# Performance work log

Hardware: AMD Instinct MI355X
Metric: run time of the kernel (lower is better)

Reference implementation:

```python
import jax, jax.numpy as jnp
import numpy as np

N = 50000      # nodes
E = 800000     # edges
G = 256        # graphs in batch
D_IN = 128     # input_dim
H = 128        # node_hidden_dim
FC = 128       # fc_hidden_dim
OUT = 2        # out_dim
EPS = 1e-5


def _lin_init(key, fan_in, fan_out, bias=True):
    kw, kb = jax.random.split(key)
    w = jax.random.normal(kw, (fan_in, fan_out), jnp.float32) / np.sqrt(fan_in)
    if bias:
        b = jax.random.normal(kb, (fan_out,), jnp.float32) * 0.01
        return w, b
    return w


def setup_inputs() -> dict:
    key = jax.random.key(0)
    ks = jax.random.split(key, 16)
    x = jax.random.normal(ks[0], (N, D_IN), jnp.float32)
    edge_index = jax.random.randint(ks[1], (2, E), 0, N, jnp.int32)
    batch = jnp.sort(jax.random.randint(ks[2], (N,), 0, G, jnp.int32))
    edge_attr = jax.random.uniform(ks[3], (E, 1), jnp.float32)
    # GraphConv params: lin_rel (with bias) + lin_root (no bias)
    w_rel1, b_rel1 = _lin_init(ks[4], D_IN, H)
    w_root1 = _lin_init(ks[5], D_IN, H, bias=False)
    w_rel2, b_rel2 = _lin_init(ks[6], H, 2 * H)
    w_root2 = _lin_init(ks[7], H, 2 * H, bias=False)
    w_rel3, b_rel3 = _lin_init(ks[8], 2 * H, 3 * H)
    w_root3 = _lin_init(ks[9], 2 * H, 3 * H, bias=False)
    # BatchNorm affine params
    gamma1 = jnp.ones((H,), jnp.float32);      beta1 = jnp.zeros((H,), jnp.float32)
    gamma2 = jnp.ones((2 * H,), jnp.float32);  beta2 = jnp.zeros((2 * H,), jnp.float32)
    gamma3 = jnp.ones((3 * H,), jnp.float32);  beta3 = jnp.zeros((3 * H,), jnp.float32)
    # FC head: lin1 in = 3H+6H+9H = 18H
    w_lin1, b_lin1 = _lin_init(ks[10], 18 * H, FC)
    w_lin2, b_lin2 = _lin_init(ks[11], FC, OUT)
    w_lin3, b_lin3 = _lin_init(ks[12], OUT, OUT)
    return dict(x=x, edge_index=edge_index, batch=batch, edge_attr=edge_attr,
                w_rel1=w_rel1, b_rel1=b_rel1, w_root1=w_root1,
                w_rel2=w_rel2, b_rel2=b_rel2, w_root2=w_root2,
                w_rel3=w_rel3, b_rel3=b_rel3, w_root3=w_root3,
                gamma1=gamma1, beta1=beta1, gamma2=gamma2, beta2=beta2,
                gamma3=gamma3, beta3=beta3,
                w_lin1=w_lin1, b_lin1=b_lin1, w_lin2=w_lin2, b_lin2=b_lin2,
                w_lin3=w_lin3, b_lin3=b_lin3)


def _bn(h, gamma, beta):
    # training-mode BatchNorm1d over node axis
    mu = h.mean(0)
    var = h.var(0)
    return (h - mu) * jax.lax.rsqrt(var + EPS) * gamma + beta


def _gconv(h, src, dst, ew, w_rel, b_rel, w_root):
    # PyG GraphConv: lin_rel(sum_j ew_ij * x_j) + lin_root(x_i)
    agg = jax.ops.segment_sum(h[src] * ew[:, None], dst, num_segments=N)
    return agg @ w_rel + b_rel + h @ w_root


def _pool3(h, batch):
    # concat of global max / mean / add pooling per graph
    s = jax.ops.segment_sum(h, batch, num_segments=G)
    cnt = jax.ops.segment_sum(jnp.ones((h.shape[0], 1), h.dtype), batch, num_segments=G)
    mean = s / jnp.maximum(cnt, 1.0)
    m = jax.ops.segment_max(h, batch, num_segments=G)
    m = jnp.where(cnt > 0, m, 0.0)  # guard empty segments
    return jnp.concatenate([m, mean, s], axis=1)


def reference(x, edge_index, batch, edge_attr,
              w_rel1, b_rel1, w_root1, w_rel2, b_rel2, w_root2,
              w_rel3, b_rel3, w_root3,
              gamma1, beta1, gamma2, beta2, gamma3, beta3,
              w_lin1, b_lin1, w_lin2, b_lin2, w_lin3, b_lin3):
    ew = jnp.transpose(edge_attr, (1, 0))[0]            # [E]
    src, dst = edge_index[0], edge_index[1]
    h = _bn(jax.nn.leaky_relu(_gconv(x, src, dst, ew, w_rel1, b_rel1, w_root1)), gamma1, beta1)
    x1 = _pool3(h, batch)
    h = _bn(jax.nn.leaky_relu(_gconv(h, src, dst, ew, w_rel2, b_rel2, w_root2)), gamma2, beta2)
    x2 = _pool3(h, batch)
    h = _bn(jax.nn.leaky_relu(_gconv(h, src, dst, ew, w_rel3, b_rel3, w_root3)), gamma3, beta3)
    x3 = _pool3(h, batch)
    z = jnp.concatenate([x1, x2, x3], axis=1)           # [G, 18H]
    z = jax.nn.relu(z @ w_lin1 + b_lin1)                # dropout is identity in eval
    z = jax.nn.relu(z @ w_lin2 + b_lin2)
    return jax.nn.log_softmax(z @ w_lin3 + b_lin3, axis=-1)
```

## Files before the change

kernel.cpp:

```cpp
#include <hip/hip_runtime.h>
#include <cstdint>
#include <cstddef>

#define N_NODES 50000
#define M_PAD   50048
#define MB_TILES 391
#define N_EDGES 800000
#define N_GRAPH 256
#define Z_DIM   2304
#define NREP    16
#define POOL_TOT (N_GRAPH * (128 + 256 + 384))

static constexpr float LEAKY  = 0.01f;
static constexpr float BN_EPS = 1e-5f;

typedef short short8 __attribute__((ext_vector_type(8)));
typedef float floatx4 __attribute__((ext_vector_type(4)));
typedef const __attribute__((address_space(1))) unsigned int* gas_ptr;
typedef __attribute__((address_space(3))) unsigned int* las_ptr;
typedef unsigned long long ull;

__device__ __forceinline__ unsigned short f2b(float f) {
  union { float f; unsigned int u; } v; v.f = f;
  unsigned int u = v.u;
  unsigned int r = (u + 0x7FFFu + ((u >> 16) & 1u)) >> 16;
  return (unsigned short)r;
}
__device__ __forceinline__ float b2f(unsigned short h) {
  union { unsigned int u; float f; } v; v.u = ((unsigned int)h) << 16;
  return v.f;
}
__device__ __forceinline__ unsigned fkey(float x) {
  unsigned k = __float_as_uint(x);
  return k ^ ((k & 0x80000000u) ? 0xFFFFFFFFu : 0x80000000u);
}
__device__ __forceinline__ float kdec(unsigned k) {
  k ^= (k & 0x80000000u) ? 0x80000000u : 0xFFFFFFFFu;
  return __uint_as_float(k);
}


__global__ void init_all_kernel(int* __restrict__ cntR, int* __restrict__ gcnt,
                                float* __restrict__ sums_all,
                                unsigned* __restrict__ pmaxk, unsigned* __restrict__ pmink,
                                float* __restrict__ psumg) {
  const int i = blockIdx.x * blockDim.x + threadIdx.x;
  if (i < NREP * N_NODES) cntR[i] = 0;
  if (i < N_GRAPH) gcnt[i] = 0;
  if (i < 2 * (128 + 256 + 384)) sums_all[i] = 0.f;
  if (i < POOL_TOT) { pmaxk[i] = 0u; pmink[i] = 0xFFFFFFFFu; psumg[i] = 0.f; }
}


__global__ void hist_rep_kernel(const int* __restrict__ idx, int* __restrict__ cntR, int n) {
  int i = blockIdx.x * blockDim.x + threadIdx.x;
  if (i < n) {
    const int rep = blockIdx.x & (NREP - 1);
    atomicAdd(&cntR[rep * N_NODES + idx[i]], 1);
  }
}

__global__ __launch_bounds__(256) void scan1_fused_kernel(int* __restrict__ cntR,
                                                          int* __restrict__ out,
                                                          int* __restrict__ part, int n) {
  __shared__ int sm[256];
  const int t = threadIdx.x;
  const int base = blockIdx.x * 1024 + t * 4;
  int v[4] = {0, 0, 0, 0};
#pragma unroll
  for (int j = 0; j < 4; ++j) {
    const int d = base + j;
    if (d < n) {
      int s = 0;
#pragma unroll
      for (int r = 0; r < NREP; ++r) {
        const int c = cntR[r * N_NODES + d];
        cntR[r * N_NODES + d] = s;
        s += c;
      }
      v[j] = s;
    }
  }
  const int tsum = v[0] + v[1] + v[2] + v[3];
  sm[t] = tsum;
  __syncthreads();
  for (int off = 1; off < 256; off <<= 1) {
    int x = (t >= off) ? sm[t - off] : 0;
    __syncthreads();
    sm[t] += x;
    __syncthreads();
  }
  const int excl = sm[t] - tsum;
  if (base     < n) out[base]     = excl;
  if (base + 1 < n) out[base + 1] = excl + v[0];
  if (base + 2 < n) out[base + 2] = excl + v[0] + v[1];
  if (base + 3 < n) out[base + 3] = excl + v[0] + v[1] + v[2];
  if (t == 255) part[blockIdx.x] = sm[255];
}

__global__ __launch_bounds__(256) void scan2_kernel(int* __restrict__ part, int nb,
                                                    int* __restrict__ total_out) {
  __shared__ int sm[256];
  const int t = threadIdx.x;
  const int v = (t < nb) ? part[t] : 0;
  sm[t] = v;
  __syncthreads();
  for (int off = 1; off < 256; off <<= 1) {
    int x = (t >= off) ? sm[t - off] : 0;
    __syncthreads();
    sm[t] += x;
    __syncthreads();
  }
  if (t < nb) part[t] = sm[t] - v;
  if (t == 255) *total_out = sm[255];
}

__global__ void scan3_cursor_kernel(int* __restrict__ out, const int* __restrict__ part,
                                    int* __restrict__ cntR, int n) {
  int i = blockIdx.x * blockDim.x + threadIdx.x;
  if (i >= n) return;
  const int rp = out[i] + part[i >> 10];
  out[i] = rp;
#pragma unroll
  for (int r = 0; r < NREP; ++r) cntR[r * N_NODES + i] += rp;
}

__global__ void bucket_kernel(const int* __restrict__ src, const int* __restrict__ dst,
                              const float* __restrict__ ew, int* __restrict__ cntR,
                              ull* __restrict__ epack, int E) {
  int e = blockIdx.x * blockDim.x + threadIdx.x;
  if (e < E) {
    const int rep = blockIdx.x & (NREP - 1);
    const int d = dst[e];
    const int p = atomicAdd(&cntR[rep * N_NODES + d], 1);
    epack[p] = ((ull)__float_as_uint(ew[e]) << 32) | (unsigned)src[e];
  }
}

__global__ __launch_bounds__(256) void hist_batch_kernel(const int* __restrict__ idx,
                                                         int* __restrict__ cnt, int n) {
  __shared__ int lh[N_GRAPH];
  lh[threadIdx.x] = 0;
  __syncthreads();
  int i = blockIdx.x * blockDim.x + threadIdx.x;
  if (i < n) atomicAdd(&lh[idx[i]], 1);
  __syncthreads();
  const int v = lh[threadIdx.x];
  if (v) atomicAdd(&cnt[threadIdx.x], v);
}

__global__ __launch_bounds__(256) void scan256_kernel(const int* __restrict__ cnt,
                                                      int* __restrict__ gptr) {
  __shared__ int sm[256];
  const int t = threadIdx.x;
  const int v = cnt[t];
  sm[t] = v;
  __syncthreads();
  for (int off = 1; off < 256; off <<= 1) {
    int x = (t >= off) ? sm[t - off] : 0;
    __syncthreads();
    sm[t] += x;
    __syncthreads();
  }
  gptr[t] = sm[t] - v;
  if (t == 255) gptr[256] = sm[255];
}


__global__ void cast_bf16_kernel(const float* __restrict__ in,
                                 unsigned short* __restrict__ out, int npair) {
  int i = blockIdx.x * blockDim.x + threadIdx.x;
  if (i >= npair) return;
  float2 v = *(const float2*)(in + 2 * (size_t)i);
  ((unsigned int*)out)[i] = (unsigned int)f2b(v.x) | ((unsigned int)f2b(v.y) << 16);
}

__global__ __launch_bounds__(256) void wt_build_kernel(
    const float* __restrict__ wrel, const float* __restrict__ wroot,
    const float* __restrict__ brel, const float* __restrict__ sums_prev,
    const float* __restrict__ gamma_prev, const float* __restrict__ beta_prev,
    unsigned short* __restrict__ wt, float* __restrict__ u, float* __restrict__ v,
    int K, int N) {
  __shared__ float redu[256];
  __shared__ float redv[256];
  const int n = blockIdx.x;
  const int K2 = 2 * K;
  const float inv_n = 1.f / (float)N_NODES;
  float us = 0.f, vs = 0.f;
  for (int k = threadIdx.x; k < K2; k += 256) {
    const int kk = (k < K) ? k : k - K;
    const float w = (k < K) ? wrel[(size_t)kk * N + n] : wroot[(size_t)kk * N + n];
    float sc = 1.f, sh = 0.f;
    if (sums_prev) {
      const float mu  = sums_prev[kk] * inv_n;
      const float var = sums_prev[K + kk] * inv_n - mu * mu;
      sc = rsqrtf(var + BN_EPS) * gamma_prev[kk];
      sh = beta_prev[kk] - mu * sc;
    }
    wt[(size_t)n * K2 + k] = f2b(w * sc);
    if (k < K) us += sh * w; else vs += sh * w;
  }
  redu[threadIdx.x] = us; redv[threadIdx.x] = vs;
  __syncthreads();
  for (int o = 128; o > 0; o >>= 1) {
    if (threadIdx.x < o) {
      redu[threadIdx.x] += redu[threadIdx.x + o];
      redv[threadIdx.x] += redv[threadIdx.x + o];
    }
    __syncthreads();
  }
  if (threadIdx.x == 0) { u[n] = redu[0]; v[n] = brel[n] + redv[0]; }
}


template <int D>
__global__ void agg_bf16_kernel(const unsigned short* __restrict__ h,
                                const int* __restrict__ rowptr,
                                const ull* __restrict__ epack,
                                unsigned short* __restrict__ agg,
                                float* __restrict__ degw_out) {
  int gid  = blockIdx.x * blockDim.x + threadIdx.x;
  int node = gid >> 6;
  int lane = threadIdx.x & 63;
  if (node >= N_NODES) return;
  const int beg = rowptr[node], end = rowptr[node + 1];
  constexpr int NP = D / 128;
  float acc0[NP], acc1[NP];
#pragma unroll
  for (int i = 0; i < NP; ++i) { acc0[i] = 0.f; acc1[i] = 0.f; }
  float wsum = 0.f;

  for (int c0 = beg; c0 < end; c0 += 64) {
    const int cn = min(64, end - c0);
    ull pk = 0;
    if (lane < cn) pk = epack[c0 + lane];
    const int   su = (int)(unsigned)pk;
    const float wf = __uint_as_float((unsigned)(pk >> 32));
    const int ng = (cn + 7) >> 3;
    for (int g = 0; g < ng; ++g) {
      int ss[8]; float wv[8];
#pragma unroll
      for (int j = 0; j < 8; ++j) {
        ss[j] = __shfl(su, g * 8 + j);
        wv[j] = __shfl(wf, g * 8 + j);
      }
      unsigned uu[8][NP];
#pragma unroll
      for (int j = 0; j < 8; ++j) {
        const unsigned int* row = (const unsigned int*)(h + (size_t)ss[j] * D);
#pragma unroll
        for (int i = 0; i < NP; ++i) uu[j][i] = row[lane + 64 * i];
      }
#pragma unroll
      for (int j = 0; j < 8; ++j) {
        wsum += wv[j];
#pragma unroll
        for (int i = 0; i < NP; ++i) {
          acc0[i] += b2f((unsigned short)(uu[j][i] & 0xFFFF)) * wv[j];
          acc1[i] += b2f((unsigned short)(uu[j][i] >> 16)) * wv[j];
        }
      }
    }
  }

  unsigned int* o = (unsigned int*)(agg + (size_t)node * D);
#pragma unroll
  for (int i = 0; i < NP; ++i)
    o[lane + 64 * i] = (unsigned int)f2b(acc0[i]) | ((unsigned int)f2b(acc1[i]) << 16);
  if (degw_out != nullptr && lane == 0) degw_out[node] = wsum;
}


__global__ __launch_bounds__(256) void gemm_mfma_kernel(
    const unsigned short* __restrict__ Aagg, const unsigned short* __restrict__ Ah,
    const unsigned short* __restrict__ Wt,
    const float* __restrict__ u, const float* __restrict__ v,
    const float* __restrict__ degw,
    unsigned short* __restrict__ outH, float* __restrict__ sums,
    int M, int K, int N) {
  __shared__ unsigned short As[3][128 * 32];
  __shared__ unsigned short Bs[3][128 * 32];
  __shared__ float col_s[256];
  __shared__ float dws[128];

  const int NT = N >> 7;
  const int id = blockIdx.x;
  const int xcd = id & 7;
  const int q   = id >> 3;
  const int m_tile = (q / NT) * 8 + xcd;
  if (m_tile >= MB_TILES) return;
  const int m0 = m_tile * 128;
  const int n0 = (q % NT) * 128;

  const int t  = threadIdx.x;
  const int lane = t & 63;
  const int w    = t >> 6;
  const int wm   = (w & 1) * 64;
  const int wn   = (w >> 1) * 64;
  const int l16  = lane & 15;
  const int lq   = lane >> 4;
  const int K2   = 2 * K;

  const int lrow  = lane >> 2;
  const int lslot = lane & 3;

  col_s[t] = 0.f;
  if (t < 128) {
    const int m = m0 + t;
    dws[t] = (m < M) ? degw[m] : 0.f;
  }

  floatx4 acc[4][4];
#pragma unroll
  for (int i = 0; i < 4; ++i)
#pragma unroll
    for (int j = 0; j < 4; ++j) acc[i][j] = (floatx4){0.f, 0.f, 0.f, 0.f};

  auto stage = [&](unsigned short* Ab, unsigned short* Bb, int k0) {
    const unsigned short* Asrc;
    int kbase;
    if (k0 < K) { Asrc = Aagg; kbase = k0; } else { Asrc = Ah; kbase = k0 - K; }
#pragma unroll
    for (int qq = 0; qq < 2; ++qq) {
      const int row = w * 32 + qq * 16 + lrow;
      const int gc  = (lslot ^ ((row >> 1) & 3)) * 8;
      const unsigned short* gA = Asrc + (size_t)(m0 + row) * K + kbase + gc;
      const unsigned short* gB = Wt + (size_t)(n0 + row) * K2 + k0 + gc;
      __builtin_amdgcn_global_load_lds((gas_ptr)gA, (las_ptr)(Ab + (w * 32 + qq * 16) * 32),
                                       16, 0, 0);
      __builtin_amdgcn_global_load_lds((gas_ptr)gB, (las_ptr)(Bb + (w * 32 + qq * 16) * 32),
                                       16, 0, 0);
    }
  };

  auto compute = [&](const unsigned short* Ab, const unsigned short* Bb) {
    short8 af[4], bfr[4];
#pragma unroll
    for (int i = 0; i < 4; ++i) {
      const int r = wm + i * 16 + l16;
      af[i] = *(const short8*)(Ab + r * 32 + (lq ^ ((r >> 1) & 3)) * 8);
    }
#pragma unroll
    for (int j = 0; j < 4; ++j) {
      const int r = wn + j * 16 + l16;
      bfr[j] = *(const short8*)(Bb + r * 32 + (lq ^ ((r >> 1) & 3)) * 8);
    }
    __builtin_amdgcn_s_setprio(1);
#pragma unroll
    for (int i = 0; i < 4; ++i)
#pragma unroll
      for (int j = 0; j < 4; ++j)
        acc[i][j] = __builtin_amdgcn_mfma_f32_16x16x32_bf16(af[i], bfr[j], acc[i][j], 0, 0, 0);
    __builtin_amdgcn_s_setprio(0);
  };

  const int NSTEP = K2 >> 5;

  unsigned short *A0 = &As[0][0], *A1 = &As[1][0], *A2 = &As[2][0];
  unsigned short *B0 = &Bs[0][0], *B1 = &Bs[1][0], *B2 = &Bs[2][0];

  stage(A0, B0, 0);
  stage(A1, B1, 1 << 5);

  for (int s = 0; s < NSTEP - 1; ++s) {
    asm volatile("s_waitcnt vmcnt(4)" ::: "memory");
    __builtin_amdgcn_s_barrier();
    __builtin_amdgcn_sched_barrier(0);
    if (s + 2 < NSTEP) stage(A2, B2, (s + 2) << 5);
    compute(A0, B0);
    unsigned short* tA = A0; A0 = A1; A1 = A2; A2 = tA;
    unsigned short* tB = B0; B0 = B1; B1 = B2; B2 = tB;
  }
  asm volatile("s_waitcnt vmcnt(0)" ::: "memory");
  __builtin_amdgcn_s_barrier();
  __builtin_amdgcn_sched_barrier(0);
  compute(A0, B0);

  float uu[4], vv[4];
#pragma unroll
  for (int j = 0; j < 4; ++j) {
    const int n = n0 + wn + j * 16 + l16;
    uu[j] = u[n]; vv[j] = v[n];
  }

  float ts[4]  = {0.f, 0.f, 0.f, 0.f};
  float tss[4] = {0.f, 0.f, 0.f, 0.f};
#pragma unroll
  for (int i = 0; i < 4; ++i) {
    const int lrow2 = wm + i * 16 + lq * 4;
#pragma unroll
    for (int j = 0; j < 4; ++j) {
      const int n = n0 + wn + j * 16 + l16;
#pragma unroll
      for (int r = 0; r < 4; ++r) {
        const int m = m0 + lrow2 + r;
        if (m < M) {
          float val = acc[i][j][r] + vv[j] + dws[lrow2 + r] * uu[j];
          val = val > 0.f ? val : LEAKY * val;
          outH[(size_t)m * N + n] = f2b(val);
          ts[j]  += val;
          tss[j] += val * val;
        }
      }
    }
  }
#pragma unroll
  for (int j = 0; j < 4; ++j) {
    float a = ts[j], b = tss[j];
    a += __shfl_xor(a, 16); a += __shfl_xor(a, 32);
    b += __shfl_xor(b, 16); b += __shfl_xor(b, 32);
    if (lq == 0) {
      const int ci = wn + j * 16 + l16;
      atomicAdd(&col_s[ci], a);
      atomicAdd(&col_s[128 + ci], b);
    }
  }
  __syncthreads();
  if (t < 128) {
    atomicAdd(&sums[n0 + t], col_s[t]);
    atomicAdd(&sums[N + n0 + t], col_s[128 + t]);
  }
}


__global__ void pool_bf16_kernel(const unsigned short* __restrict__ hp,
                                 const int* __restrict__ batch,
                                 unsigned* __restrict__ pmaxk, unsigned* __restrict__ pmink,
                                 float* __restrict__ psumg, int n, int C) {
  __shared__ int bs[64];
  const int tc = threadIdx.x;
  const int r0 = blockIdx.x * 64;
  const int r1 = min(n, r0 + 64);
  if (tc < 64 && r0 + tc < n) bs[tc] = batch[r0 + tc];
  __syncthreads();
  int cur_g = bs[0];
  float mx0 = -3.4e38f, mn0 = 3.4e38f, s0 = 0.f;
  float mx1 = -3.4e38f, mn1 = 3.4e38f, s1 = 0.f;
  for (int r = r0; r < r1; ++r) {
    const int g = bs[r - r0];
    if (g != cur_g) {
      const int c0 = 2 * tc;
      atomicMax(&pmaxk[(size_t)cur_g * C + c0], fkey(mx0));
      atomicMin(&pmink[(size_t)cur_g * C + c0], fkey(mn0));
      atomicAdd(&psumg[(size_t)cur_g * C + c0], s0);
      atomicMax(&pmaxk[(size_t)cur_g * C + c0 + 1], fkey(mx1));
      atomicMin(&pmink[(size_t)cur_g * C + c0 + 1], fkey(mn1));
      atomicAdd(&psumg[(size_t)cur_g * C + c0 + 1], s1);
      mx0 = -3.4e38f; mn0 = 3.4e38f; s0 = 0.f;
      mx1 = -3.4e38f; mn1 = 3.4e38f; s1 = 0.f;
      cur_g = g;
    }
    const unsigned uu = ((const unsigned*)(hp + (size_t)r * C))[tc];
    const float a = b2f((unsigned short)(uu & 0xFFFF));
    const float b = b2f((unsigned short)(uu >> 16));
    mx0 = fmaxf(mx0, a); mn0 = fminf(mn0, a); s0 += a;
    mx1 = fmaxf(mx1, b); mn1 = fminf(mn1, b); s1 += b;
  }
  const int c0 = 2 * tc;
  atomicMax(&pmaxk[(size_t)cur_g * C + c0], fkey(mx0));
  atomicMin(&pmink[(size_t)cur_g * C + c0], fkey(mn0));
  atomicAdd(&psumg[(size_t)cur_g * C + c0], s0);
  atomicMax(&pmaxk[(size_t)cur_g * C + c0 + 1], fkey(mx1));
  atomicMin(&pmink[(size_t)cur_g * C + c0 + 1], fkey(mn1));
  atomicAdd(&psumg[(size_t)cur_g * C + c0 + 1], s1);
}


__global__ void pool_finalize_all_kernel(const unsigned* __restrict__ pmaxk,
                                         const unsigned* __restrict__ pmink,
                                         const float* __restrict__ psumg,
                                         const float* __restrict__ sums_all,
                                         const float* __restrict__ gamma1, const float* __restrict__ beta1,
                                         const float* __restrict__ gamma2, const float* __restrict__ beta2,
                                         const float* __restrict__ gamma3, const float* __restrict__ beta3,
                                         const int* __restrict__ gptr,
                                         float* __restrict__ z) {
  int i = blockIdx.x * blockDim.x + threadIdx.x;
  if (i >= POOL_TOT) return;
  int C, zoff, li;
  const float *sums, *gamma, *beta;
  if (i < N_GRAPH * 128) {
    C = 128; zoff = 0; li = i;
    sums = sums_all; gamma = gamma1; beta = beta1;
  } else if (i < N_GRAPH * (128 + 256)) {
    C = 256; zoff = 384; li = i - N_GRAPH * 128;
    sums = sums_all + 2 * 128; gamma = gamma2; beta = beta2;
  } else {
    C = 384; zoff = 1152; li = i - N_GRAPH * (128 + 256);
    sums = sums_all + 2 * (128 + 256); gamma = gamma3; beta = beta3;
  }
  const int g = li / C, c = li % C;
  const int cnt = gptr[g + 1] - gptr[g];
  const float inv_n = 1.f / (float)N_NODES;
  const float mu  = sums[c] * inv_n;
  const float var = sums[C + c] * inv_n - mu * mu;
  const float sc  = rsqrtf(var + BN_EPS) * gamma[c];
  const float sh  = beta[c] - mu * sc;
  const float mx = kdec(pmaxk[i]);
  const float mn = kdec(pmink[i]);
  const float sm = psumg[i];
  const float zmax = (sc >= 0.f ? mx : mn) * sc + sh;
  const float zsum = sm * sc + (float)cnt * sh;
  float* zg = z + (size_t)g * Z_DIM + zoff;
  zg[c]         = (cnt > 0) ? zmax : 0.f;
  zg[C + c]     = zsum / (float)(cnt > 0 ? cnt : 1);
  zg[2 * C + c] = zsum;
}


__global__ __launch_bounds__(1024) void fc_kernel(const float* __restrict__ z,
                                                  const float* __restrict__ w1, const float* __restrict__ b1,
                                                  const float* __restrict__ w2, const float* __restrict__ b2,
                                                  const float* __restrict__ w3, const float* __restrict__ b3,
                                                  float* __restrict__ out) {
  __shared__ float zs[Z_DIM];
  __shared__ float part[8][128];
  __shared__ float h1s[128];
  __shared__ float red[128][2];
  __shared__ float y2[2];
  const int g  = blockIdx.x;
  const int t  = threadIdx.x;
  const int c  = t & 127;
  const int ks = t >> 7;
  for (int i = t; i < Z_DIM; i += 1024) zs[i] = z[(size_t)g * Z_DIM + i];
  __syncthreads();

  constexpr int KCH = Z_DIM / 8;
  const int k0 = ks * KCH;
  float acc = 0.f;
#pragma unroll 4
  for (int k = k0; k < k0 + KCH; ++k) acc += zs[k] * w1[(size_t)k * 128 + c];
  part[ks][c] = acc;
  __syncthreads();

  if (t < 128) {
    float s = b1[t];
#pragma unroll
    for (int i = 0; i < 8; ++i) s += part[i][t];
    h1s[t] = fmaxf(s, 0.f);
  }
  __syncthreads();
  if (t < 128) {
    red[t][0] = h1s[t] * w2[t * 2 + 0];
    red[t][1] = h1s[t] * w2[t * 2 + 1];
  }
  __syncthreads();
  if (t < 2) {
    float s = b2[t];
    for (int k = 0; k < 128; ++k) s += red[k][t];
    y2[t] = fmaxf(s, 0.f);
  }
  __syncthreads();
  if (t == 0) {
    const float z0 = y2[0] * w3[0] + y2[1] * w3[2] + b3[0];
    const float z1 = y2[0] * w3[1] + y2[1] * w3[3] + b3[1];
    const float m  = fmaxf(z0, z1);
    const float lse = m + logf(expf(z0 - m) + expf(z1 - m));
    out[g * 2 + 0] = z0 - lse;
    out[g * 2 + 1] = z1 - lse;
  }
}


extern "C" void kernel_launch(void* const* d_in, const int* in_sizes, int n_in,
                              void* d_out, int out_size, void* d_ws, size_t ws_size,
                              hipStream_t stream) {
  (void)in_sizes; (void)n_in; (void)out_size; (void)ws_size;
  const float* x        = (const float*)d_in[0];
  const int*   eidx     = (const int*)d_in[1];
  const int*   batch    = (const int*)d_in[2];
  const float* eattr    = (const float*)d_in[3];
  const float* w_rel1   = (const float*)d_in[4];
  const float* b_rel1   = (const float*)d_in[5];
  const float* w_root1  = (const float*)d_in[6];
  const float* w_rel2   = (const float*)d_in[7];
  const float* b_rel2   = (const float*)d_in[8];
  const float* w_root2  = (const float*)d_in[9];
  const float* w_rel3   = (const float*)d_in[10];
  const float* b_rel3   = (const float*)d_in[11];
  const float* w_root3  = (const float*)d_in[12];
  const float* gamma1   = (const float*)d_in[13];
  const float* beta1    = (const float*)d_in[14];
  const float* gamma2   = (const float*)d_in[15];
  const float* beta2    = (const float*)d_in[16];
  const float* gamma3   = (const float*)d_in[17];
  const float* beta3    = (const float*)d_in[18];
  const float* w_lin1   = (const float*)d_in[19];
  const float* b_lin1   = (const float*)d_in[20];
  const float* w_lin2   = (const float*)d_in[21];
  const float* b_lin2   = (const float*)d_in[22];
  const float* w_lin3   = (const float*)d_in[23];
  const float* b_lin3   = (const float*)d_in[24];

  const int* src = eidx;
  const int* dst = eidx + N_EDGES;
  float* outp = (float*)d_out;

  char* ws = (char*)d_ws;
  size_t off = 0;
  auto alloc = [&](size_t bytes) -> void* {
    void* p = ws + off;
    off += (bytes + 255) & ~(size_t)255;
    return p;
  };
  int*   rowptr = (int*)alloc((N_NODES + 1) * sizeof(int));
  int*   cntR   = (int*)alloc((size_t)NREP * N_NODES * sizeof(int));
  int*   gptr   = (int*)alloc((N_GRAPH + 1) * sizeof(int));
  int*   gcnt   = (int*)alloc(N_GRAPH * sizeof(int));
  int*   part   = (int*)alloc(256 * sizeof(int));
  ull*   epack  = (ull*)alloc((size_t)N_EDGES * sizeof(ull));
  float* degw   = (float*)alloc(N_NODES * sizeof(float));
  float* sums_all = (float*)alloc(2 * (128 + 256 + 384) * sizeof(float));
  float* zbuf   = (float*)alloc((size_t)N_GRAPH * Z_DIM * sizeof(float));
  unsigned* pmaxk = (unsigned*)alloc((size_t)POOL_TOT * 4);
  unsigned* pmink = (unsigned*)alloc((size_t)POOL_TOT * 4);
  float*    psumg = (float*)alloc((size_t)POOL_TOT * 4);
  unsigned short* xb   = (unsigned short*)alloc((size_t)M_PAD * 128 * 2);
  unsigned short* hp1  = (unsigned short*)alloc((size_t)M_PAD * 128 * 2);
  unsigned short* hp2  = (unsigned short*)alloc((size_t)M_PAD * 256 * 2);
  unsigned short* hp3  = (unsigned short*)alloc((size_t)M_PAD * 384 * 2);
  unsigned short* aggb = (unsigned short*)alloc((size_t)M_PAD * 256 * 2);
  unsigned short* wt1 = (unsigned short*)alloc((size_t)128 * 256 * 2);
  unsigned short* wt2 = (unsigned short*)alloc((size_t)256 * 256 * 2);
  unsigned short* wt3 = (unsigned short*)alloc((size_t)384 * 512 * 2);
  float* u1 = (float*)alloc(128 * sizeof(float));
  float* v1 = (float*)alloc(128 * sizeof(float));
  float* u2 = (float*)alloc(256 * sizeof(float));
  float* v2 = (float*)alloc(256 * sizeof(float));
  float* u3 = (float*)alloc(384 * sizeof(float));
  float* v3 = (float*)alloc(384 * sizeof(float));

  float* sums1 = sums_all;
  float* sums2 = sums_all + 2 * 128;
  float* sums3 = sums_all + 2 * (128 + 256);
  const int PO1 = 0, PO2 = N_GRAPH * 128, PO3 = N_GRAPH * (128 + 256);

  const int EB = (N_EDGES + 255) / 256;
  const int NB = (N_NODES + 255) / 256;
  const int RB = (N_NODES + 63) / 64;
  const int SB = (N_NODES + 1023) / 1024;

  init_all_kernel<<<(NREP * N_NODES + 255) / 256, 256, 0, stream>>>(
      cntR, gcnt, sums_all, pmaxk, pmink, psumg);

  hist_rep_kernel<<<EB, 256, 0, stream>>>(dst, cntR, N_EDGES);
  scan1_fused_kernel<<<SB, 256, 0, stream>>>(cntR, rowptr, part, N_NODES);
  scan2_kernel<<<1, 256, 0, stream>>>(part, SB, rowptr + N_NODES);
  scan3_cursor_kernel<<<NB, 256, 0, stream>>>(rowptr, part, cntR, N_NODES);
  bucket_kernel<<<EB, 256, 0, stream>>>(src, dst, eattr, cntR, epack, N_EDGES);

  hist_batch_kernel<<<NB, 256, 0, stream>>>(batch, gcnt, N_NODES);
  scan256_kernel<<<1, 256, 0, stream>>>(gcnt, gptr);

  cast_bf16_kernel<<<(N_NODES * 128 / 2 + 255) / 256, 256, 0, stream>>>(x, xb, N_NODES * 128 / 2);
  wt_build_kernel<<<128, 256, 0, stream>>>(w_rel1, w_root1, b_rel1, nullptr, nullptr, nullptr,
                                           wt1, u1, v1, 128, 128);

  const int aggBlocks = (N_NODES * 64 + 255) / 256;

  agg_bf16_kernel<128><<<aggBlocks, 256, 0, stream>>>(xb, rowptr, epack, aggb, degw);
  gemm_mfma_kernel<<<392 * 1, 256, 0, stream>>>(aggb, xb, wt1, u1, v1, degw,
                                                hp1, sums1, N_NODES, 128, 128);
  pool_bf16_kernel<<<RB, 64, 0, stream>>>(hp1, batch, pmaxk + PO1, pmink + PO1, psumg + PO1,
                                          N_NODES, 128);
  wt_build_kernel<<<256, 256, 0, stream>>>(w_rel2, w_root2, b_rel2, sums1, gamma1, beta1,
                                           wt2, u2, v2, 128, 256);

  agg_bf16_kernel<128><<<aggBlocks, 256, 0, stream>>>(hp1, rowptr, epack, aggb, nullptr);
  gemm_mfma_kernel<<<392 * 2, 256, 0, stream>>>(aggb, hp1, wt2, u2, v2, degw,
                                                hp2, sums2, N_NODES, 128, 256);
  pool_bf16_kernel<<<RB, 128, 0, stream>>>(hp2, batch, pmaxk + PO2, pmink + PO2, psumg + PO2,
                                           N_NODES, 256);
  wt_build_kernel<<<384, 256, 0, stream>>>(w_rel3, w_root3, b_rel3, sums2, gamma2, beta2,
                                           wt3, u3, v3, 256, 384);

  agg_bf16_kernel<256><<<aggBlocks, 256, 0, stream>>>(hp2, rowptr, epack, aggb, nullptr);
  gemm_mfma_kernel<<<392 * 3, 256, 0, stream>>>(aggb, hp2, wt3, u3, v3, degw,
                                                hp3, sums3, N_NODES, 256, 384);
  pool_bf16_kernel<<<RB, 192, 0, stream>>>(hp3, batch, pmaxk + PO3, pmink + PO3, psumg + PO3,
                                           N_NODES, 384);

  pool_finalize_all_kernel<<<(POOL_TOT + 255) / 256, 256, 0, stream>>>(
      pmaxk, pmink, psumg, sums_all, gamma1, beta1, gamma2, beta2, gamma3, beta3, gptr, zbuf);
  fc_kernel<<<N_GRAPH, 1024, 0, stream>>>(zbuf, w_lin1, b_lin1, w_lin2, b_lin2, w_lin3, b_lin3,
                                          outp);
}
```

Measured before the change: 560.0 us.

## Fuse segment max/min/sum pooling into GEMM epilogue and skip layer-3 output store

Moves the per-graph max/min/sum pooling into the GEMM epilogue. Each tile loops over the graph ids spanned by its 128 rows, reduces across lanes with shuffles, and issues atomics. This removes the three separate pool kernels and their re-read of the hidden activations. The third layer's activations are no longer written to memory at all, since only pooling and BN stats consume them. The cost is extra epilogue work per graph segment in each tile and more register pressure in the GEMM.

```diff
diff --git a/kernel.cpp b/kernel.cpp
--- a/kernel.cpp
+++ b/kernel.cpp
@@ -275,13 +275,16 @@
     const unsigned short* __restrict__ Aagg, const unsigned short* __restrict__ Ah,
     const unsigned short* __restrict__ Wt,
     const float* __restrict__ u, const float* __restrict__ v,
-    const float* __restrict__ degw,
+    const float* __restrict__ degw, const int* __restrict__ batch,
     unsigned short* __restrict__ outH, float* __restrict__ sums,
+    unsigned* __restrict__ pmaxk, unsigned* __restrict__ pmink,
+    float* __restrict__ psumg,
     int M, int K, int N) {
   __shared__ unsigned short As[3][128 * 32];
   __shared__ unsigned short Bs[3][128 * 32];
   __shared__ float col_s[256];
   __shared__ float dws[128];
+  __shared__ int gbs[128];
 
   const int NT = N >> 7;
   const int id = blockIdx.x;
@@ -308,6 +311,7 @@
   if (t < 128) {
     const int m = m0 + t;
     dws[t] = (m < M) ? degw[m] : 0.f;
+    gbs[t] = (m < M) ? batch[m] : -1;
   }
 
   floatx4 acc[4][4];
@@ -383,6 +387,7 @@
     uu[j] = u[n]; vv[j] = v[n];
   }
 
+  const bool wout = (outH != nullptr);
   float ts[4]  = {0.f, 0.f, 0.f, 0.f};
   float tss[4] = {0.f, 0.f, 0.f, 0.f};
 #pragma unroll
@@ -397,7 +402,7 @@
         if (m < M) {
           float val = acc[i][j][r] + vv[j] + dws[lrow2 + r] * uu[j];
           val = val > 0.f ? val : LEAKY * val;
-          outH[(size_t)m * N + n] = f2b(val);
+          if (wout) outH[(size_t)m * N + n] = f2b(val);
           ts[j]  += val;
           tss[j] += val * val;
         }
@@ -415,54 +420,45 @@
       atomicAdd(&col_s[128 + ci], b);
     }
   }
+
+  const int lastr = min(127, M - 1 - m0);
+  const int gmin = gbs[0];
+  const int gmax = gbs[lastr];
+  for (int g = gmin; g <= gmax; ++g) {
+#pragma unroll
+    for (int j = 0; j < 4; ++j) {
+      float mx = -3.4e38f, mn = 3.4e38f, sm = 0.f;
+#pragma unroll
+      for (int i = 0; i < 4; ++i) {
+        const int lrow2 = wm + i * 16 + lq * 4;
+#pragma unroll
+        for (int r = 0; r < 4; ++r) {
+          const int row = lrow2 + r;
+          const int m = m0 + row;
+          if (m < M && gbs[row] == g) {
+            float val = acc[i][j][r] + vv[j] + dws[row] * uu[j];
+            val = val > 0.f ? val : LEAKY * val;
+            mx = fmaxf(mx, val); mn = fminf(mn, val); sm += val;
+          }
+        }
+      }
+      mx = fmaxf(mx, __shfl_xor(mx, 16)); mx = fmaxf(mx, __shfl_xor(mx, 32));
+      mn = fminf(mn, __shfl_xor(mn, 16)); mn = fminf(mn, __shfl_xor(mn, 32));
+      sm += __shfl_xor(sm, 16); sm += __shfl_xor(sm, 32);
+      if (lq == 0 && mx > -3.3e38f) {
+        const size_t pi = (size_t)g * N + (n0 + wn + j * 16 + l16);
+        atomicMax(&pmaxk[pi], fkey(mx));
+        atomicMin(&pmink[pi], fkey(mn));
+        atomicAdd(&psumg[pi], sm);
+      }
+    }
+  }
+
   __syncthreads();
   if (t < 128) {
     atomicAdd(&sums[n0 + t], col_s[t]);
     atomicAdd(&sums[N + n0 + t], col_s[128 + t]);
   }
-}
-
-
-__global__ void pool_bf16_kernel(const unsigned short* __restrict__ hp,
-                                 const int* __restrict__ batch,
-                                 unsigned* __restrict__ pmaxk, unsigned* __restrict__ pmink,
-                                 float* __restrict__ psumg, int n, int C) {
-  __shared__ int bs[64];
-  const int tc = threadIdx.x;
-  const int r0 = blockIdx.x * 64;
-  const int r1 = min(n, r0 + 64);
-  if (tc < 64 && r0 + tc < n) bs[tc] = batch[r0 + tc];
-  __syncthreads();
-  int cur_g = bs[0];
-  float mx0 = -3.4e38f, mn0 = 3.4e38f, s0 = 0.f;
-  float mx1 = -3.4e38f, mn1 = 3.4e38f, s1 = 0.f;
-  for (int r = r0; r < r1; ++r) {
-    const int g = bs[r - r0];
-    if (g != cur_g) {
-      const int c0 = 2 * tc;
-      atomicMax(&pmaxk[(size_t)cur_g * C + c0], fkey(mx0));
-      atomicMin(&pmink[(size_t)cur_g * C + c0], fkey(mn0));
-      atomicAdd(&psumg[(size_t)cur_g * C + c0], s0);
-      atomicMax(&pmaxk[(size_t)cur_g * C + c0 + 1], fkey(mx1));
-      atomicMin(&pmink[(size_t)cur_g * C + c0 + 1], fkey(mn1));
-      atomicAdd(&psumg[(size_t)cur_g * C + c0 + 1], s1);
-      mx0 = -3.4e38f; mn0 = 3.4e38f; s0 = 0.f;
-      mx1 = -3.4e38f; mn1 = 3.4e38f; s1 = 0.f;
-      cur_g = g;
-    }
-    const unsigned uu = ((const unsigned*)(hp + (size_t)r * C))[tc];
-    const float a = b2f((unsigned short)(uu & 0xFFFF));
-    const float b = b2f((unsigned short)(uu >> 16));
-    mx0 = fmaxf(mx0, a); mn0 = fminf(mn0, a); s0 += a;
-    mx1 = fmaxf(mx1, b); mn1 = fminf(mn1, b); s1 += b;
-  }
-  const int c0 = 2 * tc;
-  atomicMax(&pmaxk[(size_t)cur_g * C + c0], fkey(mx0));
-  atomicMin(&pmink[(size_t)cur_g * C + c0], fkey(mn0));
-  atomicAdd(&psumg[(size_t)cur_g * C + c0], s0);
-  atomicMax(&pmaxk[(size_t)cur_g * C + c0 + 1], fkey(mx1));
-  atomicMin(&pmink[(size_t)cur_g * C + c0 + 1], fkey(mn1));
-  atomicAdd(&psumg[(size_t)cur_g * C + c0 + 1], s1);
 }
 
 
@@ -618,7 +614,6 @@
   unsigned short* xb   = (unsigned short*)alloc((size_t)M_PAD * 128 * 2);
   unsigned short* hp1  = (unsigned short*)alloc((size_t)M_PAD * 128 * 2);
   unsigned short* hp2  = (unsigned short*)alloc((size_t)M_PAD * 256 * 2);
-  unsigned short* hp3  = (unsigned short*)alloc((size_t)M_PAD * 384 * 2);
   unsigned short* aggb = (unsigned short*)alloc((size_t)M_PAD * 256 * 2);
   unsigned short* wt1 = (unsigned short*)alloc((size_t)128 * 256 * 2);
   unsigned short* wt2 = (unsigned short*)alloc((size_t)256 * 256 * 2);
@@ -637,7 +632,6 @@
 
   const int EB = (N_EDGES + 255) / 256;
   const int NB = (N_NODES + 255) / 256;
-  const int RB = (N_NODES + 63) / 64;
   const int SB = (N_NODES + 1023) / 1024;
 
   init_all_kernel<<<(NREP * N_NODES + 255) / 256, 256, 0, stream>>>(
@@ -659,26 +653,24 @@
   const int aggBlocks = (N_NODES * 64 + 255) / 256;
 
   agg_bf16_kernel<128><<<aggBlocks, 256, 0, stream>>>(xb, rowptr, epack, aggb, degw);
-  gemm_mfma_kernel<<<392 * 1, 256, 0, stream>>>(aggb, xb, wt1, u1, v1, degw,
-                                                hp1, sums1, N_NODES, 128, 128);
-  pool_bf16_kernel<<<RB, 64, 0, stream>>>(hp1, batch, pmaxk + PO1, pmink + PO1, psumg + PO1,
-                                          N_NODES, 128);
+  gemm_mfma_kernel<<<392 * 1, 256, 0, stream>>>(aggb, xb, wt1, u1, v1, degw, batch,
+                                                hp1, sums1, pmaxk + PO1, pmink + PO1,
+                                                psumg + PO1, N_NODES, 128, 128);
   wt_build_kernel<<<256, 256, 0, stream>>>(w_rel2, w_root2, b_rel2, sums1, gamma1, beta1,
                                            wt2, u2, v2, 128, 256);
 
   agg_bf16_kernel<128><<<aggBlocks, 256, 0, stream>>>(hp1, rowptr, epack, aggb, nullptr);
-  gemm_mfma_kernel<<<392 * 2, 256, 0, stream>>>(aggb, hp1, wt2, u2, v2, degw,
-                                                hp2, sums2, N_NODES, 128, 256);
-  pool_bf16_kernel<<<RB, 128, 0, stream>>>(hp2, batch, pmaxk + PO2, pmink + PO2, psumg + PO2,
-                                           N_NODES, 256);
+  gemm_mfma_kernel<<<392 * 2, 256, 0, stream>>>(aggb, hp1, wt2, u2, v2, degw, batch,
+                                                hp2, sums2, pmaxk + PO2, pmink + PO2,
+                                                psumg + PO2, N_NODES, 128, 256);
   wt_build_kernel<<<384, 256, 0, stream>>>(w_rel3, w_root3, b_rel3, sums2, gamma2, beta2,
                                            wt3, u3, v3, 256, 384);
 
   agg_bf16_kernel<256><<<aggBlocks, 256, 0, stream>>>(hp2, rowptr, epack, aggb, nullptr);
-  gemm_mfma_kernel<<<392 * 3, 256, 0, stream>>>(aggb, hp2, wt3, u3, v3, degw,
-                                                hp3, sums3, N_NODES, 256, 384);
-  pool_bf16_kernel<<<RB, 192, 0, stream>>>(hp3, batch, pmaxk + PO3, pmink + PO3, psumg + PO3,
-                                           N_NODES, 384);
+  gemm_mfma_kernel<<<392 * 3, 256, 0, stream>>>(aggb, hp2, wt3, u3, v3, degw, batch,
+                                                (unsigned short*)nullptr, sums3,
+                                                pmaxk + PO3, pmink + PO3, psumg + PO3,
+                                                N_NODES, 256, 384);
 
   pool_finalize_all_kernel<<<(POOL_TOT + 255) / 256, 256, 0, stream>>>(
       pmaxk, pmink, psumg, sums_all, gamma1, beta1, gamma2, beta2, gamma3, beta3, gptr, zbuf);
```

New measurement: 534.3 us. 4.6% less time.
